# Kernel tuning notes

Hardware: AMD Instinct MI355X
Metric: run time of the kernel (lower is better)

## Reference

```python
import jax, jax.numpy as jnp
import numpy as np

HEAD = 16
FEAT = 32
OUT = 32
N_E = 2048
N_UP = 1024  # n_up init kwarg (closed over; determines up/down split of x)


def _eps_ksi():
    # Complex-multiplication structure tensors (sparse 2x2x2), as in the source.
    ksi = (jnp.zeros((2, 2, 2))
           .at[0, 0, 0].set(1.0).at[1, 1, 0].set(-1.0)
           .at[0, 1, 1].set(1.0).at[1, 0, 1].set(1.0))
    eps = (jnp.zeros((2, 2, 2))
           .at[0, 0, 0].set(1.0).at[1, 1, 0].set(1.0)
           .at[0, 1, 1].set(1.0).at[1, 0, 1].set(-1.0))
    return eps, ksi


def setup_inputs() -> dict:
    key = jax.random.key(0)
    ks = jax.random.split(key, 9)
    x = jax.random.normal(ks[0], (N_E, FEAT, 3, 2), dtype=jnp.float32)
    # flax initializers.normal(1.0) -> stddev-1 normal params
    m_shape = (HEAD, FEAT, FEAT, 3, 2)
    a_shape = (HEAD, OUT, FEAT, 3, 2)
    return {
        'x': x,
        'M_uu': jax.random.normal(ks[1], m_shape, dtype=jnp.float32),
        'M_dd': jax.random.normal(ks[2], m_shape, dtype=jnp.float32),
        'M_ud': jax.random.normal(ks[3], m_shape, dtype=jnp.float32),
        'M_du': jax.random.normal(ks[4], m_shape, dtype=jnp.float32),
        'A_uu': jax.random.normal(ks[5], a_shape, dtype=jnp.float32),
        'A_dd': jax.random.normal(ks[6], a_shape, dtype=jnp.float32),
        'A_ud': jax.random.normal(ks[7], a_shape, dtype=jnp.float32),
        'A_du': jax.random.normal(ks[8], a_shape, dtype=jnp.float32),
    }


def reference(x, M_uu, M_dd, M_ud, M_du, A_uu, A_dd, A_ud, A_du):
    eps, ksi = _eps_ksi()
    u, d = x[:N_UP], x[N_UP:]  # up / down spin electrons

    def scores(q, k, M):
        # [h, n, m] attention logits, softmax over last axis (default in jax.nn.softmax)
        s = jnp.einsum('nfza,mgzb,hfgzc,abc->hnm', q, k, M, eps)
        return jax.nn.softmax(s)

    def combine(att, A, v):
        # [n, out_dims, 3, 2]
        return jnp.einsum('hnm,hgfza,mfzb,abc->ngzc', att, A, v, ksi)

    uu = scores(u, u, M_uu)
    dd = scores(d, d, M_dd)
    ud = scores(u, d, M_ud)
    du = scores(d, u, M_du)

    y_up = combine(uu, A_uu, u) + combine(ud, A_ud, d)
    y_dn = combine(dd, A_dd, d) + combine(du, A_du, u)
    return jnp.concatenate([y_up, y_dn], axis=0)  # [n_e, out_dims, 3, 2]
```

## Files before the change

### kernel.cpp

```cpp
#include <hip/hip_runtime.h>
#include <hip/hip_bf16.h>

typedef unsigned short u16;
typedef unsigned int   u32;
typedef _Float16 f16x8 __attribute__((ext_vector_type(8)));
typedef float    f32x16 __attribute__((ext_vector_type(16)));

#define HEADS 16
#define D     192
#define NUP   1024

#define XB       (2048ull*192*2)
#define XH_OFF   0ull
#define XL_OFF   (XH_OFF + XB)
#define XT_OFF   (XL_OFF + XB)
#define WM_BYTES (64ull*192*192*2)
#define WTP_OFF  (XT_OFF + XB)
#define MTH_OFF  (WTP_OFF + WM_BYTES)
#define MTL_OFF  (MTH_OFF + WM_BYTES)
#define QM_BYTES (64ull*1024*192*2)
#define QMH_OFF  (MTH_OFF + 2*WM_BYTES)
#define Y_OFF    (QMH_OFF + QM_BYTES)
#define WS_NEED  (Y_OFF + QM_BYTES)

__device__ __forceinline__ u16 f2h(float v) {
    _Float16 h = (_Float16)v;
    return __builtin_bit_cast(u16, h);
}
__device__ __forceinline__ float h2f(u16 v) {
    return (float)__builtin_bit_cast(_Float16, v);
}
__device__ __forceinline__ u32 pk2h(float a, float b) {
    return (u32)f2h(a) | ((u32)f2h(b) << 16);
}
__device__ __forceinline__ u32 pk2h_rtz(float a, float b) {
    auto r = __builtin_amdgcn_cvt_pkrtz(a, b);
    return __builtin_bit_cast(u32, r);
}

__device__ __forceinline__ f16x8 make_bfrag(u32 q0, u32 q1, u32 q2, u32 q3, bool hi) {
    u32 s0 = (u32)__shfl_xor((int)q0, 32);
    u32 s1 = (u32)__shfl_xor((int)q1, 32);
    u32 s2 = (u32)__shfl_xor((int)q2, 32);
    u32 s3 = (u32)__shfl_xor((int)q3, 32);
    uint4 w;
    w.x = hi ? s2 : q0;  w.y = hi ? s3 : q1;
    w.z = hi ? q2 : s0;  w.w = hi ? q3 : s1;
    return __builtin_bit_cast(f16x8, w);
}

__global__ __launch_bounds__(512)
void prep_all(const float* __restrict__ x,
              const float* __restrict__ Muu, const float* __restrict__ Mdd,
              const float* __restrict__ Mud, const float* __restrict__ Mdu,
              const float* __restrict__ Auu, const float* __restrict__ Add,
              const float* __restrict__ Aud, const float* __restrict__ Adu,
              u16* __restrict__ xh, u16* __restrict__ xl, u16* __restrict__ xT,
              u16* __restrict__ wtp, u16* __restrict__ mth, u16* __restrict__ mtl)
{
    int b = blockIdx.x;
    if (b < 768) {
        int i = b*512 + threadIdx.x;
        float v = x[i];
        int n = i / D, d = i - n*D;
        u16 hi = f2h(v);
        xh[i] = hi;
        xl[i] = f2h(v - h2f(hi));
        xT[(size_t)(n >> 5)*6144 + d*32 + (n & 31)] = hi;
        return;
    }
    int idx = (b - 768)*512 + threadIdx.x;
    int th = idx / 36864, r = idx - th*36864;
    int dout = r / 192, din = r - dout*192;
    int t = th >> 4, h = th & 15;
    const float* Ap = (t==0)?Auu:(t==1)?Aud:(t==2)?Add:Adu;
    const float* Mp = (t==0)?Muu:(t==1)?Mud:(t==2)?Mdd:Mdu;
    int g = dout / 6, zc = dout - g*6, z = zc >> 1, b0 = zc & 1;
    int f = din / 6,  zb = din - f*6,  z2 = zb >> 1, b1 = zb & 1;

    float wv = 0.0f, mv = 0.0f;
    if (z2 == z) {
        const float* a = Ap + (((size_t)h*32 + g)*32 + f)*6 + z*2;
        float A0 = a[0], A1 = a[1];
        wv = (b0 == 0) ? (b1 == 0 ? A0 : -A1) : (b1 == 0 ? A1 : A0);
        const float* m = Mp + (((size_t)h*32 + f)*32 + g)*6 + z*2;
        float M0 = m[0], M1 = m[1];
        mv = (b0 == 0) ? (b1 == 0 ? M0 : -M1) : (b1 == 0 ? M1 : M0);
    }
    int ob = dout >> 5, l31 = dout & 31;
    int ks = din >> 4, kr = din & 15, g32 = kr >> 3, j = kr & 7;
    size_t pidx = ((((size_t)th*6 + ob)*12 + ks)*64 + g32*32 + l31)*8 + j;
    wtp[pidx] = f2h(wv);
    u16 mh = f2h(mv);
    mth[pidx] = mh;
    mtl[pidx] = f2h(mv - h2f(mh));
}

__global__ __launch_bounds__(256, 2)
void prep_qmf2(const u16* __restrict__ xh_g, const u16* __restrict__ xl_g,
               const u16* __restrict__ mth_g, const u16* __restrict__ mtl_g,
               u16* __restrict__ qmh)
{
    const int nt = blockIdx.x, h = blockIdx.y, t = blockIdx.z;
    const int tid  = threadIdx.x;
    const int lane = tid & 63;
    const int l31  = lane & 31;
    const int g32  = lane >> 5;
    const int wave = tid >> 6;
    const int th   = t*16 + h;
    const int ntile = nt*4 + wave;
    const int n0   = ntile*32;
    const int qoff = (t <= 1) ? 0 : NUP;

    f16x8 bxh[12], bxl[12];
    const u16* xrh = xh_g + (size_t)(qoff + n0 + l31)*D;
    const u16* xrl = xl_g + (size_t)(qoff + n0 + l31)*D;
    #pragma unroll
    for (int ks = 0; ks < 12; ++ks) {
        bxh[ks] = *reinterpret_cast<const f16x8*>(xrh + ks*16 + g32*8);
        bxl[ks] = *reinterpret_cast<const f16x8*>(xrl + ks*16 + g32*8);
    }
    const u16* mthb = mth_g + (size_t)th*36864;
    const u16* mtlb = mtl_g + (size_t)th*36864;
    u16* dhrow = qmh + ((size_t)th*1024 + n0 + l31)*D + 4*g32;

    #pragma unroll
    for (int ob = 0; ob < 6; ++ob) {
        f32x16 a;
        #pragma unroll
        for (int i = 0; i < 16; ++i) a[i] = 0.0f;
        #pragma unroll
        for (int ks = 0; ks < 12; ++ks) {
            size_t fo = (((size_t)ob*12 + ks)*64 + lane)*8;
            f16x8 amh = *reinterpret_cast<const f16x8*>(mthb + fo);
            f16x8 aml = *reinterpret_cast<const f16x8*>(mtlb + fo);
            a = __builtin_amdgcn_mfma_f32_32x32x16_f16(amh, bxh[ks], a, 0, 0, 0);
            a = __builtin_amdgcn_mfma_f32_32x32x16_f16(amh, bxl[ks], a, 0, 0, 0);
            a = __builtin_amdgcn_mfma_f32_32x32x16_f16(aml, bxh[ks], a, 0, 0, 0);
        }
        #pragma unroll
        for (int q2 = 0; q2 < 4; ++q2) {
            uint2 wh;
            wh.x = pk2h(a[q2*4+0], a[q2*4+1]);
            wh.y = pk2h(a[q2*4+2], a[q2*4+3]);
            *reinterpret_cast<uint2*>(dhrow + ob*32 + q2*8) = wh;
        }
    }
}

__global__ __launch_bounds__(512, 2)
void attn_mfma(const u16* __restrict__ qmh_g, const u16* __restrict__ xh_g,
               const u16* __restrict__ xT_g,  const u16* __restrict__ wtp_g,
               u16* __restrict__ y_g)
{
    const int nt = blockIdx.x, h = blockIdx.y, t = blockIdx.z;
    const int tid  = threadIdx.x;
    const int lane = tid & 63;
    const int l31  = lane & 31;
    const int g32  = lane >> 5;
    const int th   = t*16 + h;
    const int n0   = nt*256 + (tid >> 6)*32;
    const int koff = (t == 1 || t == 2) ? NUP : 0;
    const int mtb  = koff >> 5;

    __shared__ u16 sXh[3][32*200];
    __shared__ u16 sXT[3][192*40];

    f16x8 qh[12];
    {
        const u16* bh = qmh_g + ((size_t)th*1024 + n0 + l31)*D;
        #pragma unroll
        for (int ks = 0; ks < 12; ++ks)
            qh[ks] = *reinterpret_cast<const f16x8*>(bh + ks*16 + g32*8);
    }

    f32x16 vt[6];
    #pragma unroll
    for (int ob = 0; ob < 6; ++ob)
        #pragma unroll
        for (int i = 0; i < 16; ++i) vt[ob][i] = 0.0f;

    float run_m = -3.0e38f, run_l = 0.0f;

    uint4 ld[3];
    auto load_tile = [&](int mt) {
        const int krow0 = koff + mt*32;
        #pragma unroll
        for (int i = 0; i < 3; ++i) {
            int c = tid + i*512;
            const u16* gp;
            if (c < 768) {
                int rr = c/24, cc = c - rr*24;
                gp = xh_g + (size_t)(krow0 + rr)*D + cc*8;
            } else {
                int c3 = c - 768, dd = c3 >> 2, qq = c3 & 3;
                gp = xT_g + (size_t)(mtb + mt)*6144 + dd*32 + qq*8;
            }
            ld[i] = *reinterpret_cast<const uint4*>(gp);
        }
    };
    auto store_tile = [&](int buf) {
        #pragma unroll
        for (int i = 0; i < 3; ++i) {
            int c = tid + i*512;
            u16* lp;
            if (c < 768) {
                int rr = c/24, cc = c - rr*24;  lp = &sXh[buf][rr*200 + cc*8];
            } else {
                int c3 = c - 768, dd = c3 >> 2, qq = c3 & 3;  lp = &sXT[buf][dd*40 + qq*8];
            }
            *reinterpret_cast<uint4*>(lp) = ld[i];
        }
    };
    auto SCORES = [&](int bc, f32x16 &sOut) {
        #pragma unroll
        for (int i = 0; i < 16; ++i) sOut[i] = 0.0f;
        __builtin_amdgcn_s_setprio(1);
        #pragma unroll
        for (int ks = 0; ks < 12; ++ks) {
            f16x8 ah = *reinterpret_cast<const f16x8*>(&sXh[bc][l31*200 + ks*16 + g32*8]);
            sOut = __builtin_amdgcn_mfma_f32_32x32x16_f16(ah, qh[ks], sOut, 0, 0, 0);
        }
        __builtin_amdgcn_s_setprio(0);
    };
    auto SOFTMAX = [&](f32x16 &sIn, f16x8 &pf0, f16x8 &pf1) {
        float tmax = sIn[0];
        #pragma unroll
        for (int i = 1; i < 16; ++i) tmax = fmaxf(tmax, sIn[i]);
        tmax = fmaxf(tmax, __shfl_xor(tmax, 32));
        if (__any(tmax > run_m + 8.0f)) {
            float nm = fmaxf(run_m, tmax);
            float rs = __expf(run_m - nm);
            #pragma unroll
            for (int ob = 0; ob < 6; ++ob)
                #pragma unroll
                for (int i = 0; i < 16; ++i) vt[ob][i] *= rs;
            run_l *= rs;
            run_m = nm;
        }
        float psum = 0.0f;
        u32 q[8];
        #pragma unroll
        for (int j = 0; j < 8; ++j) {
            float p0 = __expf(sIn[2*j]   - run_m);
            float p1 = __expf(sIn[2*j+1] - run_m);
            psum += p0 + p1;
            q[j] = pk2h_rtz(p0, p1);
        }
        psum += __shfl_xor(psum, 32);
        run_l += psum;
        pf0 = make_bfrag(q[0], q[1], q[2], q[3], g32);
        pf1 = make_bfrag(q[4], q[5], q[6], q[7], g32);
    };
    auto PV = [&](int bp, f16x8 pf0, f16x8 pf1) {
        __builtin_amdgcn_s_setprio(1);
        #pragma unroll
        for (int ob = 0; ob < 6; ++ob) {
            f16x8 a0 = *reinterpret_cast<const f16x8*>(&sXT[bp][(ob*32 + l31)*40 + g32*8]);
            f16x8 a1 = *reinterpret_cast<const f16x8*>(&sXT[bp][(ob*32 + l31)*40 + 16 + g32*8]);
            vt[ob] = __builtin_amdgcn_mfma_f32_32x32x16_f16(a0, pf0, vt[ob], 0, 0, 0);
            vt[ob] = __builtin_amdgcn_mfma_f32_32x32x16_f16(a1, pf1, vt[ob], 0, 0, 0);
        }
        __builtin_amdgcn_s_setprio(0);
    };

    f32x16 sA, sB;

    load_tile(0); store_tile(0); __syncthreads();
    load_tile(1);
    SCORES(0, sA);
    store_tile(1); __syncthreads();

    auto STEP = [&](int cur, f32x16 &sCur, f32x16 &sPrev, int bC, int bP, int bN) {
        if (cur < 31) load_tile(cur + 1);
        SCORES(bC, sCur);
        f16x8 pf0, pf1;
        SOFTMAX(sPrev, pf0, pf1);
        PV(bP, pf0, pf1);
        if (cur < 31) store_tile(bN);
        __syncthreads();
    };

    int b0 = 1, b1 = 0, b2 = 2;
    #pragma unroll 1
    for (int m2 = 1; m2 <= 29; m2 += 2) {
        STEP(m2,     sB, sA, b0, b1, b2);
        { int tq = b1; b1 = b0; b0 = b2; b2 = tq; }
        STEP(m2 + 1, sA, sB, b0, b1, b2);
        { int tq = b1; b1 = b0; b0 = b2; b2 = tq; }
    }
    STEP(31, sB, sA, b0, b1, b2);
    {
        f16x8 pf0, pf1;
        SOFTMAX(sB, pf0, pf1);
        PV(b0, pf0, pf1);
    }

    float inv = 1.0f / run_l;
    #pragma unroll
    for (int ob = 0; ob < 6; ++ob)
        #pragma unroll
        for (int i = 0; i < 16; ++i) vt[ob][i] *= inv;

    const u16* wbase = wtp_g + (size_t)th*36864;
    f32x16 y[6];
    #pragma unroll
    for (int ob = 0; ob < 6; ++ob)
        #pragma unroll
        for (int i = 0; i < 16; ++i) y[ob][i] = 0.0f;

    #pragma unroll
    for (int ob = 0; ob < 6; ++ob) {
        u32 qq[8];
        #pragma unroll
        for (int j = 0; j < 8; ++j) qq[j] = pk2h_rtz(vt[ob][2*j], vt[ob][2*j+1]);
        #pragma unroll
        for (int half = 0; half < 2; ++half) {
            int ks = ob*2 + half;
            f16x8 bfr = half ? make_bfrag(qq[4], qq[5], qq[6], qq[7], g32)
                             : make_bfrag(qq[0], qq[1], qq[2], qq[3], g32);
            #pragma unroll
            for (int ob2 = 0; ob2 < 6; ++ob2) {
                f16x8 a = *reinterpret_cast<const f16x8*>(
                    wbase + ((((size_t)ob2*12) + ks)*64 + lane)*8);
                y[ob2] = __builtin_amdgcn_mfma_f32_32x32x16_f16(a, bfr, y[ob2], 0, 0, 0);
            }
        }
    }

    u16* yrow = y_g + ((size_t)th*1024 + n0 + l31)*D;
    #pragma unroll
    for (int ob = 0; ob < 6; ++ob)
        #pragma unroll
        for (int rq = 0; rq < 4; ++rq) {
            uint2 v;
            v.x = pk2h_rtz(y[ob][rq*4+0], y[ob][rq*4+1]);
            v.y = pk2h_rtz(y[ob][rq*4+2], y[ob][rq*4+3]);
            *reinterpret_cast<uint2*>(yrow + ob*32 + rq*8 + g32*4) = v;
        }
}

__global__ __launch_bounds__(512)
void reduce_y(const u16* __restrict__ y_g, float* __restrict__ out)
{
    int gi = blockIdx.x*512 + threadIdx.x;
    int n = gi / 24, c = gi - n*24;
    int p = n >> 10, nn = n & 1023;
    float acc[8];
    #pragma unroll
    for (int j = 0; j < 8; ++j) acc[j] = 0.0f;
    #pragma unroll
    for (int k = 0; k < 32; ++k) {
        int tcur = p*2 + (k >> 4), hh = k & 15;
        uint4 v = *reinterpret_cast<const uint4*>(
            y_g + ((size_t)((tcur*16+hh)*1024 + nn))*D + c*8);
        u32 w[4] = {v.x, v.y, v.z, v.w};
        #pragma unroll
        for (int j = 0; j < 4; ++j) {
            acc[2*j]   += h2f((u16)(w[j] & 0xffffu));
            acc[2*j+1] += h2f((u16)(w[j] >> 16));
        }
    }
    float* op = out + (size_t)n*D + c*8;
    float4 o0 = {acc[0], acc[1], acc[2], acc[3]};
    float4 o1 = {acc[4], acc[5], acc[6], acc[7]};
    *reinterpret_cast<float4*>(op)     = o0;
    *reinterpret_cast<float4*>(op + 4) = o1;
}

__global__ __launch_bounds__(256, 2)
void attn_fused_fb(const float* __restrict__ x,
                const float* __restrict__ Muu, const float* __restrict__ Mdd,
                const float* __restrict__ Mud, const float* __restrict__ Mdu,
                const float* __restrict__ Auu, const float* __restrict__ Add,
                const float* __restrict__ Aud, const float* __restrict__ Adu,
                float* __restrict__ out)
{
    const int nt  = blockIdx.x;
    const int h   = blockIdx.y;
    const int t   = blockIdx.z;
    const int tid = threadIdx.x;
    const float* qb = (t <= 1) ? x : x + (size_t)NUP*D;
    const float* kb = (t == 0 || t == 3) ? x : x + (size_t)NUP*D;
    const float* Mp = (t==0)?Muu:(t==1)?Mud:(t==2)?Mdd:Mdu;
    const float* Ap = (t==0)?Auu:(t==1)?Aud:(t==2)?Add:Adu;
    const float* Mh = Mp + (size_t)h*32*D;
    const float* Ah = Ap + (size_t)h*32*D;
    float* ob = out + ((t>=2) ? (size_t)NUP*D : 0);

    __shared__ float sK[32*196];
    __shared__ float sQM[32*196];
    __shared__ float sS[32*33];
    __shared__ float sTmp[32*8];
    __shared__ float sR[32];
    __shared__ float sMaxRun[32];
    __shared__ float sSumRun[32];

    if (tid < 32) { sMaxRun[tid] = -3.0e38f; sSumRun[tid] = 0.0f; }
    for (int i = tid; i < 32*D/4; i += 256)
        reinterpret_cast<float4*>(sK)[i] = reinterpret_cast<const float4*>(Mh)[i];
    __syncthreads();

    #pragma unroll
    for (int kk = 0; kk < 4; ++kk) {
        int p = tid + kk*256;
        int n = p >> 5, g = p & 31;
        const float* qrow = qb + (size_t)(nt*32 + n)*D;
        float acc[6] = {0,0,0,0,0,0};
        for (int f = 0; f < 32; ++f) {
            const float* qf = qrow + f*6;
            const float* mf = sK + f*D + g*6;
            #pragma unroll
            for (int z = 0; z < 3; ++z) {
                float q0 = qf[2*z], q1 = qf[2*z+1];
                float m0 = mf[2*z], m1 = mf[2*z+1];
                acc[2*z]   += q0*m0 - q1*m1;
                acc[2*z+1] += q1*m0 + q0*m1;
            }
        }
        #pragma unroll
        for (int j = 0; j < 6; ++j) sQM[n*196 + g*6 + j] = acc[j];
    }

    const int gn = tid >> 5;
    const int cg = tid & 31;
    const int cbase = cg*6;
    float vacc[4][6];
    #pragma unroll
    for (int a = 0; a < 4; ++a)
        #pragma unroll
        for (int b = 0; b < 6; ++b) vacc[a][b] = 0.0f;

    const int txm = tid & 15, tyn = tid >> 4;

    for (int mt = 0; mt < 32; ++mt) {
        __syncthreads();
        for (int i = tid; i < 32*(D/4); i += 256) {
            int row = i / (D/4), j = i - row*(D/4);
            float4 v = reinterpret_cast<const float4*>(kb + (size_t)(mt*32 + row)*D)[j];
            *reinterpret_cast<float4*>(&sK[row*196 + j*4]) = v;
        }
        __syncthreads();

        float a00=0,a01=0,a10=0,a11=0;
        {
            const float* q0p = &sQM[tyn*196];
            const float* q1p = &sQM[(tyn+16)*196];
            const float* k0p = &sK[txm*196];
            const float* k1p = &sK[(txm+16)*196];
            for (int k = 0; k < D; k += 4) {
                float4 qa = *reinterpret_cast<const float4*>(q0p+k);
                float4 qc = *reinterpret_cast<const float4*>(q1p+k);
                float4 ka = *reinterpret_cast<const float4*>(k0p+k);
                float4 kc = *reinterpret_cast<const float4*>(k1p+k);
                a00 += qa.x*ka.x + qa.y*ka.y + qa.z*ka.z + qa.w*ka.w;
                a01 += qa.x*kc.x + qa.y*kc.y + qa.z*kc.z + qa.w*kc.w;
                a10 += qc.x*ka.x + qc.y*ka.y + qc.z*ka.z + qc.w*ka.w;
                a11 += qc.x*kc.x + qc.y*kc.y + qc.z*kc.z + qc.w*kc.w;
            }
        }
        sS[tyn*33 + txm]          = a00;
        sS[tyn*33 + txm+16]       = a01;
        sS[(tyn+16)*33 + txm]     = a10;
        sS[(tyn+16)*33 + txm+16]  = a11;
        __syncthreads();

        const int srow = tid >> 3, sj = tid & 7;
        {
            const float* r = &sS[srow*33];
            float mx = fmaxf(fmaxf(r[sj], r[sj+8]), fmaxf(r[sj+16], r[sj+24]));
            sTmp[srow*8 + sj] = mx;
        }
        __syncthreads();
        if (tid < 32) {
            float mx = sTmp[tid*8];
            #pragma unroll
            for (int j = 1; j < 8; ++j) mx = fmaxf(mx, sTmp[tid*8+j]);
            float om = sMaxRun[tid];
            float nm = fmaxf(om, mx);
            sR[tid] = __expf(om - nm);
            sMaxRun[tid] = nm;
        }
        __syncthreads();
        {
            float nm = sMaxRun[srow];
            float* r = &sS[srow*33];
            float p0 = __expf(r[sj]    - nm);
            float p1 = __expf(r[sj+8]  - nm);
            float p2 = __expf(r[sj+16] - nm);
            float p3 = __expf(r[sj+24] - nm);
            r[sj] = p0; r[sj+8] = p1; r[sj+16] = p2; r[sj+24] = p3;
            sTmp[srow*8+sj] = p0+p1+p2+p3;
        }
        __syncthreads();
        if (tid < 32) {
            float s = 0.0f;
            #pragma unroll
            for (int j = 0; j < 8; ++j) s += sTmp[tid*8+j];
            sSumRun[tid] = sSumRun[tid]*sR[tid] + s;
        }
        {
            float r0 = sR[gn*4+0], r1 = sR[gn*4+1], r2 = sR[gn*4+2], r3 = sR[gn*4+3];
            #pragma unroll
            for (int b = 0; b < 6; ++b) { vacc[0][b]*=r0; vacc[1][b]*=r1; vacc[2][b]*=r2; vacc[3][b]*=r3; }
            for (int m = 0; m < 32; ++m) {
                float p0 = sS[(gn*4+0)*33+m];
                float p1 = sS[(gn*4+1)*33+m];
                float p2 = sS[(gn*4+2)*33+m];
                float p3 = sS[(gn*4+3)*33+m];
                const float* kr = &sK[m*196 + cbase];
                #pragma unroll
                for (int b = 0; b < 6; ++b) {
                    float kv = kr[b];
                    vacc[0][b] += p0*kv;
                    vacc[1][b] += p1*kv;
                    vacc[2][b] += p2*kv;
                    vacc[3][b] += p3*kv;
                }
            }
        }
    }

    __syncthreads();
    {
        float i0 = 1.0f/sSumRun[gn*4+0], i1 = 1.0f/sSumRun[gn*4+1];
        float i2 = 1.0f/sSumRun[gn*4+2], i3 = 1.0f/sSumRun[gn*4+3];
        #pragma unroll
        for (int b = 0; b < 6; ++b) {
            sQM[(gn*4+0)*196 + cbase + b] = vacc[0][b]*i0;
            sQM[(gn*4+1)*196 + cbase + b] = vacc[1][b]*i1;
            sQM[(gn*4+2)*196 + cbase + b] = vacc[2][b]*i2;
            sQM[(gn*4+3)*196 + cbase + b] = vacc[3][b]*i3;
        }
    }
    for (int i = tid; i < 32*D/4; i += 256)
        reinterpret_cast<float4*>(sK)[i] = reinterpret_cast<const float4*>(Ah)[i];
    __syncthreads();

    #pragma unroll
    for (int kk = 0; kk < 4; ++kk) {
        int p = tid + kk*256;
        int n = p >> 5, g = p & 31;
        float acc[6] = {0,0,0,0,0,0};
        const float* vb = &sQM[n*196];
        const float* ab = &sK[g*D];
        for (int f = 0; f < 32; ++f) {
            const float* vf = vb + f*6;
            const float* af = ab + f*6;
            #pragma unroll
            for (int z = 0; z < 3; ++z) {
                float V0 = vf[2*z], V1 = vf[2*z+1];
                float A0 = af[2*z], A1 = af[2*z+1];
                acc[2*z]   += A0*V0 - A1*V1;
                acc[2*z+1] += A0*V1 + A1*V0;
            }
        }
        float* op = ob + (size_t)(nt*32 + n)*D + g*6;
        #pragma unroll
        for (int j = 0; j < 6; ++j) atomicAdd(op + j, acc[j]);
    }
}

extern "C" void kernel_launch(void* const* d_in, const int* in_sizes, int n_in,
                              void* d_out, int out_size, void* d_ws, size_t ws_size,
                              hipStream_t stream) {
    const float* x   = (const float*)d_in[0];
    const float* Muu = (const float*)d_in[1];
    const float* Mdd = (const float*)d_in[2];
    const float* Mud = (const float*)d_in[3];
    const float* Mdu = (const float*)d_in[4];
    const float* Auu = (const float*)d_in[5];
    const float* Add = (const float*)d_in[6];
    const float* Aud = (const float*)d_in[7];
    const float* Adu = (const float*)d_in[8];
    float* outp = (float*)d_out;

    if (ws_size >= WS_NEED) {
        char* ws = (char*)d_ws;
        u16* xh  = (u16*)(ws + XH_OFF);
        u16* xl  = (u16*)(ws + XL_OFF);
        u16* xT  = (u16*)(ws + XT_OFF);
        u16* wtp = (u16*)(ws + WTP_OFF);
        u16* mth = (u16*)(ws + MTH_OFF);
        u16* mtl = (u16*)(ws + MTL_OFF);
        u16* qmh = (u16*)(ws + QMH_OFF);
        u16* y   = (u16*)(ws + Y_OFF);

        prep_all<<<5376, 512, 0, stream>>>(x, Muu, Mdd, Mud, Mdu,
                                           Auu, Add, Aud, Adu,
                                           xh, xl, xT, wtp, mth, mtl);
        prep_qmf2<<<dim3(8, 16, 4), 256, 0, stream>>>(xh, xl, mth, mtl, qmh);
        attn_mfma<<<dim3(4, 16, 4), 512, 0, stream>>>(qmh, xh, xT, wtp, y);
        reduce_y<<<96, 512, 0, stream>>>(y, outp);
    } else {
        (void)hipMemsetAsync(d_out, 0, (size_t)out_size * sizeof(float), stream);
        attn_fused_fb<<<dim3(32, 16, 4), 256, 0, stream>>>(x, Muu, Mdd, Mud, Mdu,
                                                           Auu, Add, Aud, Adu, outp);
    }
}
```

Before: 151.9 us.

## Fuse Q·M projection into attention kernel and split score accumulation chains

Removes the separate prep_qmf2 kernel and computes the projected query fragments directly inside attn_mfma, converting the MFMA accumulators into B-fragments in registers with cross-lane shuffles instead of writing qmh to global memory and reading it back. The projection interleaves two output blocks so independent MFMA chains overlap. The score loop is also split into two independent accumulators that are summed afterwards, to shorten the dependent MFMA chain. This saves one launch and a large global round trip, but adds register pressure and prologue work in a kernel already limited to 512 threads with 2 blocks per CU.

```diff
diff --git a/kernel.cpp b/kernel.cpp
--- a/kernel.cpp
+++ b/kernel.cpp
@@ -18,10 +18,9 @@
 #define WTP_OFF  (XT_OFF + XB)
 #define MTH_OFF  (WTP_OFF + WM_BYTES)
 #define MTL_OFF  (MTH_OFF + WM_BYTES)
-#define QM_BYTES (64ull*1024*192*2)
-#define QMH_OFF  (MTH_OFF + 2*WM_BYTES)
-#define Y_OFF    (QMH_OFF + QM_BYTES)
-#define WS_NEED  (Y_OFF + QM_BYTES)
+#define Y_BYTES  (64ull*1024*192*2)
+#define Y_OFF    (MTH_OFF + 2*WM_BYTES)
+#define WS_NEED  (Y_OFF + Y_BYTES)
 
 __device__ __forceinline__ u16 f2h(float v) {
     _Float16 h = (_Float16)v;
@@ -96,61 +95,10 @@
     mtl[pidx] = f2h(mv - h2f(mh));
 }
 
-__global__ __launch_bounds__(256, 2)
-void prep_qmf2(const u16* __restrict__ xh_g, const u16* __restrict__ xl_g,
+__global__ __launch_bounds__(512, 2)
+void attn_mfma(const u16* __restrict__ xh_g,  const u16* __restrict__ xl_g,
+               const u16* __restrict__ xT_g,  const u16* __restrict__ wtp_g,
                const u16* __restrict__ mth_g, const u16* __restrict__ mtl_g,
-               u16* __restrict__ qmh)
-{
-    const int nt = blockIdx.x, h = blockIdx.y, t = blockIdx.z;
-    const int tid  = threadIdx.x;
-    const int lane = tid & 63;
-    const int l31  = lane & 31;
-    const int g32  = lane >> 5;
-    const int wave = tid >> 6;
-    const int th   = t*16 + h;
-    const int ntile = nt*4 + wave;
-    const int n0   = ntile*32;
-    const int qoff = (t <= 1) ? 0 : NUP;
-
-    f16x8 bxh[12], bxl[12];
-    const u16* xrh = xh_g + (size_t)(qoff + n0 + l31)*D;
-    const u16* xrl = xl_g + (size_t)(qoff + n0 + l31)*D;
-    #pragma unroll
-    for (int ks = 0; ks < 12; ++ks) {
-        bxh[ks] = *reinterpret_cast<const f16x8*>(xrh + ks*16 + g32*8);
-        bxl[ks] = *reinterpret_cast<const f16x8*>(xrl + ks*16 + g32*8);
-    }
-    const u16* mthb = mth_g + (size_t)th*36864;
-    const u16* mtlb = mtl_g + (size_t)th*36864;
-    u16* dhrow = qmh + ((size_t)th*1024 + n0 + l31)*D + 4*g32;
-
-    #pragma unroll
-    for (int ob = 0; ob < 6; ++ob) {
-        f32x16 a;
-        #pragma unroll
-        for (int i = 0; i < 16; ++i) a[i] = 0.0f;
-        #pragma unroll
-        for (int ks = 0; ks < 12; ++ks) {
-            size_t fo = (((size_t)ob*12 + ks)*64 + lane)*8;
-            f16x8 amh = *reinterpret_cast<const f16x8*>(mthb + fo);
-            f16x8 aml = *reinterpret_cast<const f16x8*>(mtlb + fo);
-            a = __builtin_amdgcn_mfma_f32_32x32x16_f16(amh, bxh[ks], a, 0, 0, 0);
-            a = __builtin_amdgcn_mfma_f32_32x32x16_f16(amh, bxl[ks], a, 0, 0, 0);
-            a = __builtin_amdgcn_mfma_f32_32x32x16_f16(aml, bxh[ks], a, 0, 0, 0);
-        }
-        #pragma unroll
-        for (int q2 = 0; q2 < 4; ++q2) {
-            uint2 wh;
-            wh.x = pk2h(a[q2*4+0], a[q2*4+1]);
-            wh.y = pk2h(a[q2*4+2], a[q2*4+3]);
-            *reinterpret_cast<uint2*>(dhrow + ob*32 + q2*8) = wh;
-        }
-    }
-}
-
-__global__ __launch_bounds__(512, 2)
-void attn_mfma(const u16* __restrict__ qmh_g, const u16* __restrict__ xh_g,
-               const u16* __restrict__ xT_g,  const u16* __restrict__ wtp_g,
                u16* __restrict__ y_g)
 {
     const int nt = blockIdx.x, h = blockIdx.y, t = blockIdx.z;
@@ -160,6 +108,7 @@
     const int g32  = lane >> 5;
     const int th   = t*16 + h;
     const int n0   = nt*256 + (tid >> 6)*32;
+    const int qoff = (t <= 1) ? 0 : NUP;
     const int koff = (t == 1 || t == 2) ? NUP : 0;
     const int mtb  = koff >> 5;
 
@@ -168,10 +117,48 @@
 
     f16x8 qh[12];
     {
-        const u16* bh = qmh_g + ((size_t)th*1024 + n0 + l31)*D;
-        #pragma unroll
-        for (int ks = 0; ks < 12; ++ks)
-            qh[ks] = *reinterpret_cast<const f16x8*>(bh + ks*16 + g32*8);
+        f16x8 bxh[12], bxl[12];
+        const u16* xrh = xh_g + (size_t)(qoff + n0 + l31)*D;
+        const u16* xrl = xl_g + (size_t)(qoff + n0 + l31)*D;
+        #pragma unroll
+        for (int ks = 0; ks < 12; ++ks) {
+            bxh[ks] = *reinterpret_cast<const f16x8*>(xrh + ks*16 + g32*8);
+            bxl[ks] = *reinterpret_cast<const f16x8*>(xrl + ks*16 + g32*8);
+        }
+        const u16* mthb = mth_g + (size_t)th*36864;
+        const u16* mtlb = mtl_g + (size_t)th*36864;
+        #pragma unroll
+        for (int obp = 0; obp < 3; ++obp) {
+            const int ob0 = obp*2, ob1 = obp*2 + 1;
+            f32x16 a0, a1;
+            #pragma unroll
+            for (int i = 0; i < 16; ++i) { a0[i] = 0.0f; a1[i] = 0.0f; }
+            #pragma unroll
+            for (int ks = 0; ks < 12; ++ks) {
+                size_t fo0 = (((size_t)ob0*12 + ks)*64 + lane)*8;
+                size_t fo1 = (((size_t)ob1*12 + ks)*64 + lane)*8;
+                f16x8 amh0 = *reinterpret_cast<const f16x8*>(mthb + fo0);
+                f16x8 aml0 = *reinterpret_cast<const f16x8*>(mtlb + fo0);
+                f16x8 amh1 = *reinterpret_cast<const f16x8*>(mthb + fo1);
+                f16x8 aml1 = *reinterpret_cast<const f16x8*>(mtlb + fo1);
+                a0 = __builtin_amdgcn_mfma_f32_32x32x16_f16(amh0, bxh[ks], a0, 0, 0, 0);
+                a1 = __builtin_amdgcn_mfma_f32_32x32x16_f16(amh1, bxh[ks], a1, 0, 0, 0);
+                a0 = __builtin_amdgcn_mfma_f32_32x32x16_f16(amh0, bxl[ks], a0, 0, 0, 0);
+                a1 = __builtin_amdgcn_mfma_f32_32x32x16_f16(amh1, bxl[ks], a1, 0, 0, 0);
+                a0 = __builtin_amdgcn_mfma_f32_32x32x16_f16(aml0, bxh[ks], a0, 0, 0, 0);
+                a1 = __builtin_amdgcn_mfma_f32_32x32x16_f16(aml1, bxh[ks], a1, 0, 0, 0);
+            }
+            u32 h0[8], h1[8];
+            #pragma unroll
+            for (int j = 0; j < 8; ++j) {
+                h0[j] = pk2h(a0[2*j], a0[2*j+1]);
+                h1[j] = pk2h(a1[2*j], a1[2*j+1]);
+            }
+            qh[ob0*2+0] = make_bfrag(h0[0], h0[1], h0[2], h0[3], g32);
+            qh[ob0*2+1] = make_bfrag(h0[4], h0[5], h0[6], h0[7], g32);
+            qh[ob1*2+0] = make_bfrag(h1[0], h1[1], h1[2], h1[3], g32);
+            qh[ob1*2+1] = make_bfrag(h1[4], h1[5], h1[6], h1[7], g32);
+        }
     }
 
     f32x16 vt[6];
@@ -213,15 +200,20 @@
         }
     };
     auto SCORES = [&](int bc, f32x16 &sOut) {
-        #pragma unroll
-        for (int i = 0; i < 16; ++i) sOut[i] = 0.0f;
+        f32x16 s0, s1;
+        #pragma unroll
+        for (int i = 0; i < 16; ++i) { s0[i] = 0.0f; s1[i] = 0.0f; }
         __builtin_amdgcn_s_setprio(1);
         #pragma unroll
-        for (int ks = 0; ks < 12; ++ks) {
-            f16x8 ah = *reinterpret_cast<const f16x8*>(&sXh[bc][l31*200 + ks*16 + g32*8]);
-            sOut = __builtin_amdgcn_mfma_f32_32x32x16_f16(ah, qh[ks], sOut, 0, 0, 0);
+        for (int ks = 0; ks < 6; ++ks) {
+            f16x8 ah0 = *reinterpret_cast<const f16x8*>(&sXh[bc][l31*200 + ks*16 + g32*8]);
+            f16x8 ah1 = *reinterpret_cast<const f16x8*>(&sXh[bc][l31*200 + (ks+6)*16 + g32*8]);
+            s0 = __builtin_amdgcn_mfma_f32_32x32x16_f16(ah0, qh[ks],   s0, 0, 0, 0);
+            s1 = __builtin_amdgcn_mfma_f32_32x32x16_f16(ah1, qh[ks+6], s1, 0, 0, 0);
         }
         __builtin_amdgcn_s_setprio(0);
+        #pragma unroll
+        for (int i = 0; i < 16; ++i) sOut[i] = s0[i] + s1[i];
     };
     auto SOFTMAX = [&](f32x16 &sIn, f16x8 &pf0, f16x8 &pf1) {
         float tmax = sIn[0];
@@ -583,14 +575,12 @@
         u16* wtp = (u16*)(ws + WTP_OFF);
         u16* mth = (u16*)(ws + MTH_OFF);
         u16* mtl = (u16*)(ws + MTL_OFF);
-        u16* qmh = (u16*)(ws + QMH_OFF);
         u16* y   = (u16*)(ws + Y_OFF);
 
         prep_all<<<5376, 512, 0, stream>>>(x, Muu, Mdd, Mud, Mdu,
                                            Auu, Add, Aud, Adu,
                                            xh, xl, xT, wtp, mth, mtl);
-        prep_qmf2<<<dim3(8, 16, 4), 256, 0, stream>>>(xh, xl, mth, mtl, qmh);
-        attn_mfma<<<dim3(4, 16, 4), 512, 0, stream>>>(qmh, xh, xT, wtp, y);
+        attn_mfma<<<dim3(4, 16, 4), 512, 0, stream>>>(xh, xl, xT, wtp, mth, mtl, y);
         reduce_y<<<96, 512, 0, stream>>>(y, outp);
     } else {
         (void)hipMemsetAsync(d_out, 0, (size_t)out_size * sizeof(float), stream);
```

Result: faster. 128.2 us, median of 2 (-15.6%).
